# Kernel optimization log

Measured on AMD Instinct MI355X. Metric: run time of the kernel, lower is better.

Reference implementation:

```python
import jax, jax.numpy as jnp
import numpy as np

N_HEADS = 12
HEAD_DIM = 64
EMB_DIM = 768
ATTN_DIM = N_HEADS * HEAD_DIM


def setup_inputs() -> dict:
    key = jax.random.key(0)
    k1, k2, k3, k4 = jax.random.split(key, 4)
    B, N = 8, 1024
    x = jax.random.normal(k1, (B, N, EMB_DIM), dtype=jnp.float32)
    scale = 1.0 / np.sqrt(EMB_DIM)
    w_qkv = jax.random.normal(k2, (EMB_DIM, 3 * ATTN_DIM), dtype=jnp.float32) * scale
    w_out = jax.random.normal(k3, (ATTN_DIM, EMB_DIM), dtype=jnp.float32) * (1.0 / np.sqrt(ATTN_DIM))
    b_out = jax.random.normal(k4, (EMB_DIM,), dtype=jnp.float32) * 0.01
    return {"x": x, "w_qkv": w_qkv, "w_out": w_out, "b_out": b_out}


def reference(x, w_qkv, w_out, b_out):
    B, N, _ = x.shape
    qkv = jnp.einsum('bnd,de->bne', x, w_qkv)  # [B,N,3*attn_dim]
    q, k, v = jnp.split(qkv, 3, axis=-1)
    # [B, n_heads, N, head_dim]
    def heads(t):
        return t.reshape(B, N, N_HEADS, HEAD_DIM).transpose(0, 2, 1, 3)
    q, k, v = heads(q), heads(k), heads(v)
    scores = jnp.einsum('bhnd,bhmd->bhnm', q, k) * (HEAD_DIM ** -0.5)
    attn = jax.nn.softmax(scores, axis=-1)
    out = jnp.einsum('bhnm,bhmd->bhnd', attn, v)
    out = out.transpose(0, 2, 1, 3).reshape(B, N, ATTN_DIM)
    return jnp.einsum('bnd,de->bne', out, w_out) + b_out
```

## Files before the change

### kernel.cpp

```cpp
#include <hip/hip_runtime.h>
#include <hip/hip_bf16.h>

typedef unsigned short u16;
typedef __attribute__((ext_vector_type(8))) short short8;
typedef __attribute__((ext_vector_type(4))) float floatx4;

#define SEQ    1024
#define EMB    768
#define NHEADS 12
#define HDIM   64
#define QKVD   2304
#define BATCH  8
#define ROWS   8192
#define QKW    1536

__device__ __forceinline__ u16 f2bf(float f) {
  unsigned int x; __builtin_memcpy(&x, &f, 4);
  x = (x + 0x7FFFu + ((x >> 16) & 1u)) >> 16;
  return (u16)x;
}
__device__ __forceinline__ unsigned int pack2bf_t(float a, float b) {
  unsigned int ua, ub;
  __builtin_memcpy(&ua, &a, 4); __builtin_memcpy(&ub, &b, 4);
  return (ub & 0xFFFF0000u) | (ua >> 16);
}

__device__ __forceinline__ void gld16(const void* g, void* l) {
  __builtin_amdgcn_global_load_lds(
      (const __attribute__((address_space(1))) void*)g,
      (__attribute__((address_space(3))) void*)l, 16, 0, 0);
}

#define PIPE_BARRIER_VM(N) asm volatile("s_waitcnt vmcnt(" #N ")\n\ts_barrier" ::: "memory")
#define PIPE_BARRIER       asm volatile("s_barrier" ::: "memory")

__global__ __launch_bounds__(256) void prep(const float* __restrict__ x,
                                            const float* __restrict__ wqkv,
                                            const float* __restrict__ wout,
                                            u16* __restrict__ xb,
                                            u16* __restrict__ dqkv,
                                            u16* __restrict__ dout) {
  const int t = threadIdx.x;
  if (blockIdx.x < 3072) {
    const int i = (blockIdx.x * 256 + t) * 8;
    u16 tmp[8];
#pragma unroll
    for (int j = 0; j < 8; ++j) tmp[j] = f2bf(x[i + j]);
    *(uint4*)(xb + i) = *(const uint4*)tmp;
    return;
  }
  __shared__ u16 tile[32][33];
  const int bid = blockIdx.x - 3072;
  const int bx = bid % 96, by = bid / 96;
  const bool second = bx >= 72;
  const float* in = second ? wout : wqkv;
  u16* out = second ? dout : dqkv;
  const int C = second ? EMB : QKVD;
  const int c0 = (second ? bx - 72 : bx) * 32, r0 = by * 32;
  const int tx = t & 31, ty = t >> 5;
#pragma unroll
  for (int i = 0; i < 4; ++i)
    tile[ty + i * 8][tx] = f2bf(in[(size_t)(r0 + ty + i * 8) * C + c0 + tx]);
  __syncthreads();
#pragma unroll
  for (int i = 0; i < 4; ++i)
    out[(size_t)(c0 + ty + i * 8) * EMB + r0 + tx] = tile[tx][ty + i * 8];
}

__global__ __launch_bounds__(256) void gemm_qkv(const u16* __restrict__ A,
                                                const u16* __restrict__ Bt,
                                                u16* __restrict__ qk,
                                                u16* __restrict__ vT) {
  constexpr int K = EMB, ITERS = K / 64;
  __shared__ __align__(16) u16 As[2][128 * 64];
  __shared__ __align__(16) u16 Bs[2][128 * 64];
  const int t = threadIdx.x;
  const int w = t >> 6, lane = t & 63, l16 = lane & 15, quad = lane >> 4;
  const int wm = (w >> 1) * 64, wn = (w & 1) * 64;
  const int flat = blockIdx.y * 18 + blockIdx.x;
  const int grp = flat / 144, loc = flat % 144;
  const int m0 = (grp * 8 + (loc & 7)) * 128;
  const int n0 = (loc >> 3) * 128;

  auto stage = [&](int k0, int buf) {
#pragma unroll
    for (int i = 0; i < 4; ++i) {
      const int idx = i * 256 + t;
      const int row = idx >> 3;
      const int gc8 = (((idx & 7) ^ (row & 7)) << 3);
      gld16(A  + (size_t)(m0 + row) * K + k0 + gc8, &As[buf][(size_t)idx * 8]);
      gld16(Bt + (size_t)(n0 + row) * K + k0 + gc8, &Bs[buf][(size_t)idx * 8]);
    }
  };

  floatx4 acc[4][4];
#pragma unroll
  for (int mt = 0; mt < 4; ++mt)
#pragma unroll
    for (int nt = 0; nt < 4; ++nt) acc[mt][nt] = (floatx4){0.f, 0.f, 0.f, 0.f};

  stage(0, 0);
  for (int it = 0; it < ITERS; ++it) {
    const int cur = it & 1;
    if (it + 1 < ITERS) {
      stage((it + 1) * 64, cur ^ 1);
      PIPE_BARRIER_VM(8);
    } else {
      PIPE_BARRIER_VM(0);
    }
#pragma unroll
    for (int kk = 0; kk < 2; ++kk) {
      short8 a[4], b[4];
#pragma unroll
      for (int mt = 0; mt < 4; ++mt) {
        const int row = wm + mt * 16 + l16;
        a[mt] = *(const short8*)(&As[cur][row * 64 + ((((kk << 2) + quad) ^ (row & 7)) << 3)]);
      }
#pragma unroll
      for (int nt = 0; nt < 4; ++nt) {
        const int row = wn + nt * 16 + l16;
        b[nt] = *(const short8*)(&Bs[cur][row * 64 + ((((kk << 2) + quad) ^ (row & 7)) << 3)]);
      }
#pragma unroll
      for (int mt = 0; mt < 4; ++mt)
#pragma unroll
        for (int nt = 0; nt < 4; ++nt)
          acc[mt][nt] = __builtin_amdgcn_mfma_f32_16x16x32_bf16(a[mt], b[nt], acc[mt][nt], 0, 0, 0);
    }
    PIPE_BARRIER;
  }

  if (n0 < QKW) {
#pragma unroll
    for (int mt = 0; mt < 4; ++mt)
#pragma unroll
      for (int nt = 0; nt < 4; ++nt) {
        const int col = n0 + wn + nt * 16 + l16;
#pragma unroll
        for (int r = 0; r < 4; ++r) {
          const int row = m0 + wm + mt * 16 + quad * 4 + r;
          qk[(size_t)row * QKW + col] = f2bf(acc[mt][nt][r]);
        }
      }
  } else {
#pragma unroll
    for (int mt = 0; mt < 4; ++mt) {
      const int rowb = m0 + wm + mt * 16 + quad * 4;
      const int b = rowb >> 10, n = rowb & 1023;
#pragma unroll
      for (int nt = 0; nt < 4; ++nt) {
        const int vc = n0 + wn + nt * 16 + l16 - QKW;
        const int h = vc >> 6, d = vc & 63;
        ushort4 pk;
        pk.x = f2bf(acc[mt][nt][0]); pk.y = f2bf(acc[mt][nt][1]);
        pk.z = f2bf(acc[mt][nt][2]); pk.w = f2bf(acc[mt][nt][3]);
        *(ushort4*)(vT + ((size_t)(b * NHEADS + h) * HDIM + d) * SEQ + n) = pk;
      }
    }
  }
}

__global__ __launch_bounds__(256) void flash_attn(const u16* __restrict__ qk,
                                                  const u16* __restrict__ vT,
                                                  u16* __restrict__ aout) {
  __shared__ __align__(16) u16 QPs[128 * 64];
  __shared__ __align__(16) u16 Ks[3][32 * 64];
  __shared__ __align__(16) u16 Vs[3][64 * 32];

  const int t = threadIdx.x;
  const int w = t >> 6, lane = t & 63, l16 = lane & 15, quad = lane >> 4;
  const int bh = blockIdx.x, b = bh / NHEADS, h = bh % NHEADS;
  const int m0 = blockIdx.y * 128;
  constexpr float C_EXP = 0.125f * 1.44269504f;
  constexpr int ITERS = SEQ / 32;

  const size_t kbase = (size_t)(b * SEQ) * QKW + EMB + h * HDIM;
  const size_t vbase = (size_t)bh * HDIM * SEQ;

  auto stage = [&](int n0, int buf) {
    const int kr = t >> 3, ck = t & 7;
    gld16(qk + kbase + (size_t)(n0 + kr) * QKW + ((ck ^ (kr & 7)) << 3),
          &Ks[buf][(size_t)t * 8]);
    const int dr = t >> 2, cv = t & 3;
    gld16(vT + vbase + (size_t)dr * SEQ + n0 + ((cv ^ (dr & 3)) << 3),
          &Vs[buf][(size_t)t * 8]);
  };

  stage(0, 0);
  stage(32, 1);

  const size_t qbase = (size_t)(b * SEQ + m0) * QKW + h * HDIM;
#pragma unroll
  for (int i = 0; i < 4; ++i) {
    const int idx = i * 256 + t, row = idx >> 3, c = idx & 7;
    *(uint4*)(QPs + row * 64 + ((c ^ (row & 7)) << 3)) =
        *(const uint4*)(qk + qbase + (size_t)row * QKW + (c << 3));
  }
  __syncthreads();

  short8 bq[2][2];
#pragma unroll
  for (int mt = 0; mt < 2; ++mt)
#pragma unroll
    for (int kc = 0; kc < 2; ++kc)
      bq[mt][kc] = *(const short8*)(QPs + (w * 32 + mt * 16 + l16) * 64 +
                                    ((((kc << 2) + quad) ^ (l16 & 7)) << 3));

  short8 ones;
#pragma unroll
  for (int j = 0; j < 8; ++j) ones[j] = (short)0x3F80;

  floatx4 o[2][4], lcc[2];
#pragma unroll
  for (int mt = 0; mt < 2; ++mt) {
    lcc[mt] = (floatx4){0.f, 0.f, 0.f, 0.f};
#pragma unroll
    for (int ct = 0; ct < 4; ++ct) o[mt][ct] = (floatx4){0.f, 0.f, 0.f, 0.f};
  }

  u16* Pw = QPs + w * 32 * 64;

  int cur = 0;
  for (int it = 0; it < ITERS; ++it) {
    int nxt = cur + 2; if (nxt >= 3) nxt -= 3;
    if (it + 2 < ITERS) {
      stage((it + 2) * 32, nxt);
      PIPE_BARRIER_VM(4);
    } else if (it + 1 < ITERS) {
      PIPE_BARRIER_VM(2);
    } else {
      PIPE_BARRIER_VM(0);
    }

    floatx4 st[2][2];
#pragma unroll
    for (int kt = 0; kt < 2; ++kt)
#pragma unroll
      for (int mt = 0; mt < 2; ++mt) st[kt][mt] = (floatx4){0.f, 0.f, 0.f, 0.f};
#pragma unroll
    for (int kt = 0; kt < 2; ++kt) {
      const int krow = (kt * 16 + l16) * 64;
      const short8 ak0 = *(const short8*)(&Ks[cur][krow + (((0 + quad) ^ (l16 & 7)) << 3)]);
      const short8 ak1 = *(const short8*)(&Ks[cur][krow + (((4 + quad) ^ (l16 & 7)) << 3)]);
#pragma unroll
      for (int mt = 0; mt < 2; ++mt) {
        st[kt][mt] = __builtin_amdgcn_mfma_f32_16x16x32_bf16(ak0, bq[mt][0], st[kt][mt], 0, 0, 0);
        st[kt][mt] = __builtin_amdgcn_mfma_f32_16x16x32_bf16(ak1, bq[mt][1], st[kt][mt], 0, 0, 0);
      }
    }

#pragma unroll
    for (int mt = 0; mt < 2; ++mt)
#pragma unroll
      for (int kt = 0; kt < 2; ++kt) {
        const float p0 = __builtin_amdgcn_exp2f(st[kt][mt][0] * C_EXP);
        const float p1 = __builtin_amdgcn_exp2f(st[kt][mt][1] * C_EXP);
        const float p2 = __builtin_amdgcn_exp2f(st[kt][mt][2] * C_EXP);
        const float p3 = __builtin_amdgcn_exp2f(st[kt][mt][3] * C_EXP);
        uint2 pw2;
        pw2.x = pack2bf_t(p0, p1);
        pw2.y = pack2bf_t(p2, p3);
        *(uint2*)(Pw + (mt * 16 + l16) * 64 +
                  ((((kt << 1) + (quad >> 1)) ^ (l16 & 7)) << 3) + ((quad & 1) << 2)) = pw2;
      }

#pragma unroll
    for (int mt = 0; mt < 2; ++mt) {
      const short8 ap = *(const short8*)(Pw + (mt * 16 + l16) * 64 +
                                        ((quad ^ (l16 & 7)) << 3));
      lcc[mt] = __builtin_amdgcn_mfma_f32_16x16x32_bf16(ap, ones, lcc[mt], 0, 0, 0);
#pragma unroll
      for (int ct = 0; ct < 4; ++ct) {
        const short8 bv = *(const short8*)(&Vs[cur][(ct * 16 + l16) * 32 +
                                                    ((quad ^ (l16 & 3)) << 3)]);
        o[mt][ct] = __builtin_amdgcn_mfma_f32_16x16x32_bf16(ap, bv, o[mt][ct], 0, 0, 0);
      }
    }
    PIPE_BARRIER;
    cur = (cur + 1 == 3) ? 0 : cur + 1;
  }

#pragma unroll
  for (int mt = 0; mt < 2; ++mt) {
    floatx4 inv;
#pragma unroll
    for (int r = 0; r < 4; ++r) inv[r] = 1.f / lcc[mt][r];
#pragma unroll
    for (int ct = 0; ct < 4; ++ct)
#pragma unroll
      for (int r = 0; r < 4; ++r) {
        const int row = m0 + w * 32 + mt * 16 + quad * 4 + r;
        const int col = h * HDIM + ct * 16 + l16;
        aout[(size_t)(b * SEQ + row) * EMB + col] = f2bf(o[mt][ct][r] * inv[r]);
      }
  }
}

__global__ __launch_bounds__(256) void gemm_out(const u16* __restrict__ A,
                                                const u16* __restrict__ Bt,
                                                const float* __restrict__ bias,
                                                float* __restrict__ C) {
  constexpr int K = EMB, N = EMB, ITERS = K / 64;
  __shared__ __align__(16) u16 As[2][64 * 64];
  __shared__ __align__(16) u16 Bs[2][128 * 64];
  const int t = threadIdx.x;
  const int w = t >> 6, lane = t & 63, l16 = lane & 15, quad = lane >> 4;
  const int wm = (w >> 1) * 32, wn = (w & 1) * 64;
  const int flat = blockIdx.y * 6 + blockIdx.x;
  const int grp = flat / 48, loc = flat % 48;
  const int m0 = (grp * 8 + (loc & 7)) * 64;
  const int n0 = (loc >> 3) * 128;

  auto stage = [&](int k0, int buf) {
#pragma unroll
    for (int i = 0; i < 2; ++i) {
      const int idx = i * 256 + t;
      const int row = idx >> 3;
      const int gc8 = (((idx & 7) ^ (row & 7)) << 3);
      gld16(A + (size_t)(m0 + row) * K + k0 + gc8, &As[buf][(size_t)idx * 8]);
    }
#pragma unroll
    for (int i = 0; i < 4; ++i) {
      const int idx = i * 256 + t;
      const int row = idx >> 3;
      const int gc8 = (((idx & 7) ^ (row & 7)) << 3);
      gld16(Bt + (size_t)(n0 + row) * K + k0 + gc8, &Bs[buf][(size_t)idx * 8]);
    }
  };

  floatx4 acc[2][4];
#pragma unroll
  for (int mt = 0; mt < 2; ++mt)
#pragma unroll
    for (int nt = 0; nt < 4; ++nt) acc[mt][nt] = (floatx4){0.f, 0.f, 0.f, 0.f};

  stage(0, 0);
  for (int it = 0; it < ITERS; ++it) {
    const int cur = it & 1;
    if (it + 1 < ITERS) {
      stage((it + 1) * 64, cur ^ 1);
      PIPE_BARRIER_VM(6);
    } else {
      PIPE_BARRIER_VM(0);
    }
#pragma unroll
    for (int kk = 0; kk < 2; ++kk) {
      short8 a[2], b[4];
#pragma unroll
      for (int mt = 0; mt < 2; ++mt) {
        const int row = wm + mt * 16 + l16;
        a[mt] = *(const short8*)(&As[cur][row * 64 + ((((kk << 2) + quad) ^ (row & 7)) << 3)]);
      }
#pragma unroll
      for (int nt = 0; nt < 4; ++nt) {
        const int row = wn + nt * 16 + l16;
        b[nt] = *(const short8*)(&Bs[cur][row * 64 + ((((kk << 2) + quad) ^ (row & 7)) << 3)]);
      }
#pragma unroll
      for (int mt = 0; mt < 2; ++mt)
#pragma unroll
        for (int nt = 0; nt < 4; ++nt)
          acc[mt][nt] = __builtin_amdgcn_mfma_f32_16x16x32_bf16(a[mt], b[nt], acc[mt][nt], 0, 0, 0);
    }
    PIPE_BARRIER;
  }

#pragma unroll
  for (int mt = 0; mt < 2; ++mt)
#pragma unroll
    for (int nt = 0; nt < 4; ++nt) {
      const int col = n0 + wn + nt * 16 + l16;
      const float badd = bias[col];
#pragma unroll
      for (int r = 0; r < 4; ++r) {
        const int row = m0 + wm + mt * 16 + quad * 4 + r;
        C[(size_t)row * N + col] = acc[mt][nt][r] + badd;
      }
    }
}

extern "C" void kernel_launch(void* const* d_in, const int* in_sizes, int n_in,
                              void* d_out, int out_size, void* d_ws, size_t ws_size,
                              hipStream_t stream) {
  const float* x     = (const float*)d_in[0];
  const float* w_qkv = (const float*)d_in[1];
  const float* w_out = (const float*)d_in[2];
  const float* b_out = (const float*)d_in[3];
  float* out = (float*)d_out;

  u16* qk    = (u16*)d_ws;
  u16* vT    = qk    + (size_t)ROWS * QKW;
  u16* xb    = vT    + (size_t)BATCH * NHEADS * HDIM * SEQ;
  u16* aout  = xb;
  u16* wqkvT = xb    + (size_t)ROWS * EMB;
  u16* woutT = wqkvT + (size_t)QKVD * EMB;

  prep<<<3072 + 2304, 256, 0, stream>>>(x, w_qkv, w_out, xb, wqkvT, woutT);

  gemm_qkv<<<dim3(18, 64), 256, 0, stream>>>(xb, wqkvT, qk, vT);

  flash_attn<<<dim3(BATCH * NHEADS, SEQ / 128), 256, 0, stream>>>(qk, vT, aout);

  gemm_out<<<dim3(6, 128), 256, 0, stream>>>(aout, woutT, b_out, out);
}
```

Measured before the change: 187.2 us.

## Keep softmax P in registers, widen KV tile to 64, fold scale into Q

```diff
diff --git a/kernel.cpp b/kernel.cpp
--- a/kernel.cpp
+++ b/kernel.cpp
@@ -131,6 +131,7 @@
   }
 
   if (n0 < QKW) {
+    const float qs = (n0 < EMB) ? 0.1803368801111f : 1.0f;
 #pragma unroll
     for (int mt = 0; mt < 4; ++mt)
 #pragma unroll
@@ -139,7 +140,7 @@
 #pragma unroll
         for (int r = 0; r < 4; ++r) {
           const int row = m0 + wm + mt * 16 + quad * 4 + r;
-          qk[(size_t)row * QKW + col] = f2bf(acc[mt][nt][r]);
+          qk[(size_t)row * QKW + col] = f2bf(acc[mt][nt][r] * qs);
         }
       }
   } else {
@@ -163,118 +164,110 @@
 __global__ __launch_bounds__(256) void flash_attn(const u16* __restrict__ qk,
                                                   const u16* __restrict__ vT,
                                                   u16* __restrict__ aout) {
-  __shared__ __align__(16) u16 QPs[128 * 64];
-  __shared__ __align__(16) u16 Ks[3][32 * 64];
-  __shared__ __align__(16) u16 Vs[3][64 * 32];
+  __shared__ __align__(16) u16 Ks[3][64 * 64];
+  __shared__ __align__(16) u16 Vs[3][64 * 64];
 
   const int t = threadIdx.x;
   const int w = t >> 6, lane = t & 63, l16 = lane & 15, quad = lane >> 4;
   const int bh = blockIdx.x, b = bh / NHEADS, h = bh % NHEADS;
   const int m0 = blockIdx.y * 128;
-  constexpr float C_EXP = 0.125f * 1.44269504f;
-  constexpr int ITERS = SEQ / 32;
+  constexpr int ITERS = SEQ / 64;
+  const int swz = l16 & 7;
 
   const size_t kbase = (size_t)(b * SEQ) * QKW + EMB + h * HDIM;
   const size_t vbase = (size_t)bh * HDIM * SEQ;
 
   auto stage = [&](int n0, int buf) {
-    const int kr = t >> 3, ck = t & 7;
-    gld16(qk + kbase + (size_t)(n0 + kr) * QKW + ((ck ^ (kr & 7)) << 3),
-          &Ks[buf][(size_t)t * 8]);
-    const int dr = t >> 2, cv = t & 3;
-    gld16(vT + vbase + (size_t)dr * SEQ + n0 + ((cv ^ (dr & 3)) << 3),
-          &Vs[buf][(size_t)t * 8]);
+#pragma unroll
+    for (int i = 0; i < 2; ++i) {
+      const int idx = i * 256 + t, r = idx >> 3;
+      const int gc = (((idx & 7) ^ (r & 7)) << 3);
+      gld16(qk + kbase + (size_t)(n0 + r) * QKW + gc, &Ks[buf][(size_t)idx * 8]);
+      gld16(vT + vbase + (size_t)r * SEQ + n0 + gc,   &Vs[buf][(size_t)idx * 8]);
+    }
   };
 
+  short8 bq[2][2];
+  const u16* qrow = qk + (size_t)(b * SEQ + m0 + w * 32 + l16) * QKW + h * HDIM;
+#pragma unroll
+  for (int mt = 0; mt < 2; ++mt)
+#pragma unroll
+    for (int kc = 0; kc < 2; ++kc)
+      bq[mt][kc] = *(const short8*)(qrow + (size_t)mt * 16 * QKW + kc * 32 + quad * 8);
+
   stage(0, 0);
-  stage(32, 1);
-
-  const size_t qbase = (size_t)(b * SEQ + m0) * QKW + h * HDIM;
-#pragma unroll
-  for (int i = 0; i < 4; ++i) {
-    const int idx = i * 256 + t, row = idx >> 3, c = idx & 7;
-    *(uint4*)(QPs + row * 64 + ((c ^ (row & 7)) << 3)) =
-        *(const uint4*)(qk + qbase + (size_t)row * QKW + (c << 3));
-  }
-  __syncthreads();
-
-  short8 bq[2][2];
-#pragma unroll
-  for (int mt = 0; mt < 2; ++mt)
-#pragma unroll
-    for (int kc = 0; kc < 2; ++kc)
-      bq[mt][kc] = *(const short8*)(QPs + (w * 32 + mt * 16 + l16) * 64 +
-                                    ((((kc << 2) + quad) ^ (l16 & 7)) << 3));
+  stage(64, 1);
 
   short8 ones;
 #pragma unroll
   for (int j = 0; j < 8; ++j) ones[j] = (short)0x3F80;
+  const floatx4 zf = (floatx4){0.f, 0.f, 0.f, 0.f};
 
   floatx4 o[2][4], lcc[2];
 #pragma unroll
   for (int mt = 0; mt < 2; ++mt) {
-    lcc[mt] = (floatx4){0.f, 0.f, 0.f, 0.f};
-#pragma unroll
-    for (int ct = 0; ct < 4; ++ct) o[mt][ct] = (floatx4){0.f, 0.f, 0.f, 0.f};
-  }
-
-  u16* Pw = QPs + w * 32 * 64;
+    lcc[mt] = zf;
+#pragma unroll
+    for (int dt = 0; dt < 4; ++dt) o[mt][dt] = zf;
+  }
 
   int cur = 0;
   for (int it = 0; it < ITERS; ++it) {
     int nxt = cur + 2; if (nxt >= 3) nxt -= 3;
     if (it + 2 < ITERS) {
-      stage((it + 2) * 32, nxt);
+      stage((it + 2) * 64, nxt);
+      PIPE_BARRIER_VM(8);
+    } else if (it + 1 < ITERS) {
       PIPE_BARRIER_VM(4);
-    } else if (it + 1 < ITERS) {
-      PIPE_BARRIER_VM(2);
     } else {
       PIPE_BARRIER_VM(0);
     }
 
-    floatx4 st[2][2];
-#pragma unroll
-    for (int kt = 0; kt < 2; ++kt)
-#pragma unroll
-      for (int mt = 0; mt < 2; ++mt) st[kt][mt] = (floatx4){0.f, 0.f, 0.f, 0.f};
-#pragma unroll
-    for (int kt = 0; kt < 2; ++kt) {
+    floatx4 st[4][2];
+#pragma unroll
+    for (int kt = 0; kt < 4; ++kt) {
       const int krow = (kt * 16 + l16) * 64;
-      const short8 ak0 = *(const short8*)(&Ks[cur][krow + (((0 + quad) ^ (l16 & 7)) << 3)]);
-      const short8 ak1 = *(const short8*)(&Ks[cur][krow + (((4 + quad) ^ (l16 & 7)) << 3)]);
+      const short8 ak0 = *(const short8*)(&Ks[cur][krow + ((0 ^ (quad ^ swz)) << 3) + ((quad ^ swz) == (quad ^ swz) ? 0 : 0)]);
+      const short8 ak1 = *(const short8*)(&Ks[cur][krow + (((4 + quad) ^ swz) << 3)]);
+      const short8 ak0f = *(const short8*)(&Ks[cur][krow + ((quad ^ swz) << 3)]);
 #pragma unroll
       for (int mt = 0; mt < 2; ++mt) {
-        st[kt][mt] = __builtin_amdgcn_mfma_f32_16x16x32_bf16(ak0, bq[mt][0], st[kt][mt], 0, 0, 0);
+        st[kt][mt] = __builtin_amdgcn_mfma_f32_16x16x32_bf16(ak0f, bq[mt][0], zf, 0, 0, 0);
         st[kt][mt] = __builtin_amdgcn_mfma_f32_16x16x32_bf16(ak1, bq[mt][1], st[kt][mt], 0, 0, 0);
       }
-    }
-
+      (void)ak0;
+    }
+
+    union { uint4 u; short8 s; } bp[2][2];
 #pragma unroll
     for (int mt = 0; mt < 2; ++mt)
 #pragma unroll
-      for (int kt = 0; kt < 2; ++kt) {
-        const float p0 = __builtin_amdgcn_exp2f(st[kt][mt][0] * C_EXP);
-        const float p1 = __builtin_amdgcn_exp2f(st[kt][mt][1] * C_EXP);
-        const float p2 = __builtin_amdgcn_exp2f(st[kt][mt][2] * C_EXP);
-        const float p3 = __builtin_amdgcn_exp2f(st[kt][mt][3] * C_EXP);
-        uint2 pw2;
-        pw2.x = pack2bf_t(p0, p1);
-        pw2.y = pack2bf_t(p2, p3);
-        *(uint2*)(Pw + (mt * 16 + l16) * 64 +
-                  ((((kt << 1) + (quad >> 1)) ^ (l16 & 7)) << 3) + ((quad & 1) << 2)) = pw2;
-      }
-
-#pragma unroll
-    for (int mt = 0; mt < 2; ++mt) {
-      const short8 ap = *(const short8*)(Pw + (mt * 16 + l16) * 64 +
-                                        ((quad ^ (l16 & 7)) << 3));
-      lcc[mt] = __builtin_amdgcn_mfma_f32_16x16x32_bf16(ap, ones, lcc[mt], 0, 0, 0);
-#pragma unroll
-      for (int ct = 0; ct < 4; ++ct) {
-        const short8 bv = *(const short8*)(&Vs[cur][(ct * 16 + l16) * 32 +
-                                                    ((quad ^ (l16 & 3)) << 3)]);
-        o[mt][ct] = __builtin_amdgcn_mfma_f32_16x16x32_bf16(ap, bv, o[mt][ct], 0, 0, 0);
-      }
+      for (int ktp = 0; ktp < 2; ++ktp) {
+        const floatx4 e0 = st[2 * ktp][mt], e1 = st[2 * ktp + 1][mt];
+        bp[ktp][mt].u.x = pack2bf_t(__builtin_amdgcn_exp2f(e0[0]), __builtin_amdgcn_exp2f(e0[1]));
+        bp[ktp][mt].u.y = pack2bf_t(__builtin_amdgcn_exp2f(e0[2]), __builtin_amdgcn_exp2f(e0[3]));
+        bp[ktp][mt].u.z = pack2bf_t(__builtin_amdgcn_exp2f(e1[0]), __builtin_amdgcn_exp2f(e1[1]));
+        bp[ktp][mt].u.w = pack2bf_t(__builtin_amdgcn_exp2f(e1[2]), __builtin_amdgcn_exp2f(e1[3]));
+      }
+
+#pragma unroll
+    for (int ktp = 0; ktp < 2; ++ktp) {
+      const int gl = 4 * ktp + (quad >> 1), ho = (quad & 1) * 4;
+#pragma unroll
+      for (int dt = 0; dt < 4; ++dt) {
+        const int row = dt * 16 + l16;
+        const u16* vr = &Vs[cur][row * 64];
+        union { uint4 u; short8 s; } av;
+        const uint2 lo = *(const uint2*)(vr + ((gl ^ swz) << 3) + ho);
+        const uint2 hi = *(const uint2*)(vr + (((gl + 2) ^ swz) << 3) + ho);
+        av.u.x = lo.x; av.u.y = lo.y; av.u.z = hi.x; av.u.w = hi.y;
+#pragma unroll
+        for (int mt = 0; mt < 2; ++mt)
+          o[mt][dt] = __builtin_amdgcn_mfma_f32_16x16x32_bf16(av.s, bp[ktp][mt].s, o[mt][dt], 0, 0, 0);
+      }
+#pragma unroll
+      for (int mt = 0; mt < 2; ++mt)
+        lcc[mt] = __builtin_amdgcn_mfma_f32_16x16x32_bf16(ones, bp[ktp][mt].s, lcc[mt], 0, 0, 0);
     }
     PIPE_BARRIER;
     cur = (cur + 1 == 3) ? 0 : cur + 1;
@@ -282,17 +275,15 @@
 
 #pragma unroll
   for (int mt = 0; mt < 2; ++mt) {
-    floatx4 inv;
-#pragma unroll
-    for (int r = 0; r < 4; ++r) inv[r] = 1.f / lcc[mt][r];
-#pragma unroll
-    for (int ct = 0; ct < 4; ++ct)
-#pragma unroll
-      for (int r = 0; r < 4; ++r) {
-        const int row = m0 + w * 32 + mt * 16 + quad * 4 + r;
-        const int col = h * HDIM + ct * 16 + l16;
-        aout[(size_t)(b * SEQ + row) * EMB + col] = f2bf(o[mt][ct][r] * inv[r]);
-      }
+    const float inv = 1.f / lcc[mt][0];
+    const size_t arow = (size_t)(b * SEQ + m0 + w * 32 + mt * 16 + l16) * EMB + h * HDIM;
+#pragma unroll
+    for (int dt = 0; dt < 4; ++dt) {
+      ushort4 pk;
+      pk.x = f2bf(o[mt][dt][0] * inv); pk.y = f2bf(o[mt][dt][1] * inv);
+      pk.z = f2bf(o[mt][dt][2] * inv); pk.w = f2bf(o[mt][dt][3] * inv);
+      *(ushort4*)(aout + arow + dt * 16 + quad * 4) = pk;
+    }
   }
 }
 
```

Measured after the change: 183.7 us. About the same (-1.9%).
